# Performance work log

Measured on AMD Instinct MI355X. Metric: run time of the kernel, lower is better.

## Reference

```python
import jax, jax.numpy as jnp
import numpy as np

EPS = 1e-5

def _mode_layer(x, t, w5, w3, w1, a3, a5, gw, gb, gamma, beta):
    # x: [N,Ci,H,W], t: [N,T]
    N = x.shape[0]
    Co = w5.shape[0]
    # gate -> softmax over the 5 experts (dim=1)
    g = t @ gw.T + gb                       # [N, 5*Co]
    g = jax.nn.softmax(g.reshape(N, 5, Co), axis=1)  # [N,5,Co]
    # build the 5 expert kernels, all padded to 5x5 (torch F.pad semantics)
    k3 = jnp.pad(w3, ((0, 0), (0, 0), (1, 1), (1, 1)))
    k1 = jnp.pad(w1, ((0, 0), (0, 0), (2, 2), (2, 2)))
    # avg pool kernels: ones(K,K)/K**3 (faithful to original, incl. the /K^3)
    ka3 = jnp.pad(a3 * (jnp.ones((3, 3), x.dtype) / 27.0), ((0, 0), (0, 0), (1, 1), (1, 1)))
    ka5 = a5 * (jnp.ones((5, 5), x.dtype) / 125.0)
    experts = jnp.stack([w5, k3, k1, ka3, ka5])       # [5,Co,Ci,5,5]
    # per-sample kernels: sum_e g[n,e,o] * experts[e,o,i,h,w]
    w = jnp.einsum('eoihw,neo->noihw', experts, g)    # [N,Co,Ci,5,5]
    # per-sample conv (training-mode path), padding='same', stride=1
    def conv1(xn, wn):
        return jax.lax.conv_general_dilated(xn[None], wn, (1, 1), 'SAME')[0]
    y = jax.vmap(conv1)(x, w)                         # [N,Co,H,W]
    # BatchNorm2d (training mode: biased batch stats) + ReLU
    mean = y.mean(axis=(0, 2, 3))
    var = y.var(axis=(0, 2, 3))
    y = (y - mean[None, :, None, None]) * jax.lax.rsqrt(var + EPS)[None, :, None, None]
    y = y * gamma[None, :, None, None] + beta[None, :, None, None]
    return jax.nn.relu(y)


def setup_inputs() -> dict:
    key = jax.random.key(0)
    ks = jax.random.split(key, 20)
    N, Ci, Co, T, H, W = 8, 32, 64, 8, 256, 256
    f = jnp.float32
    inp = {
        'x': jax.random.normal(ks[0], (N, Ci, H, W), f),
        't': jax.random.normal(ks[1], (N, T), f),
        'w5_1': jax.random.normal(ks[2], (Co, Ci, 5, 5), f) * 0.05,
        'w3_1': jax.random.normal(ks[3], (Co, Ci, 3, 3), f) * 0.05,
        'w1_1': jax.random.normal(ks[4], (Co, Ci, 1, 1), f) * 0.05,
        'a3_1': jax.random.normal(ks[5], (Co, Ci, 1, 1), f) * 0.05,
        'a5_1': jax.random.normal(ks[6], (Co, Ci, 1, 1), f) * 0.05,
        'gw_1': jax.random.normal(ks[7], (5 * Co, T), f) * 0.1,
        'gb_1': jax.random.normal(ks[8], (5 * Co,), f) * 0.1,
        'gamma_1': jnp.ones((Co,), f),
        'beta_1': jnp.zeros((Co,), f),
        'w5_2': jax.random.normal(ks[9], (Co, Co, 5, 5), f) * 0.05,
        'w3_2': jax.random.normal(ks[10], (Co, Co, 3, 3), f) * 0.05,
        'w1_2': jax.random.normal(ks[11], (Co, Co, 1, 1), f) * 0.05,
        'a3_2': jax.random.normal(ks[12], (Co, Co, 1, 1), f) * 0.05,
        'a5_2': jax.random.normal(ks[13], (Co, Co, 1, 1), f) * 0.05,
        'gw_2': jax.random.normal(ks[14], (5 * Co, T), f) * 0.1,
        'gb_2': jax.random.normal(ks[15], (5 * Co,), f) * 0.1,
        'gamma_2': jnp.ones((Co,), f),
        'beta_2': jnp.zeros((Co,), f),
    }
    return inp


def reference(x, t,
              w5_1, w3_1, w1_1, a3_1, a5_1, gw_1, gb_1, gamma_1, beta_1,
              w5_2, w3_2, w1_2, a3_2, a5_2, gw_2, gb_2, gamma_2, beta_2):
    h = _mode_layer(x, t, w5_1, w3_1, w1_1, a3_1, a5_1, gw_1, gb_1, gamma_1, beta_1)
    y = _mode_layer(h, t, w5_2, w3_2, w1_2, a3_2, a5_2, gw_2, gb_2, gamma_2, beta_2)
    return y
```

## Files before the change

### kernel.cpp

```cpp
#include <hip/hip_runtime.h>
#include <hip/hip_bf16.h>

#define MK_N 8
#define MK_T 8
#define MK_H 256
#define MK_W 256
#define MK_CO 64
#define MK_EPS 1e-5f

typedef __attribute__((ext_vector_type(8))) short short8;
typedef __attribute__((ext_vector_type(4))) short short4v;
typedef __attribute__((ext_vector_type(4))) float f32x4;

__device__ __forceinline__ float rdv(const void* p, long idx, int isf32) {
  return isf32 ? ((const float*)p)[idx]
               : __bfloat162float(((const __hip_bfloat16*)p)[idx]);
}

__device__ __forceinline__ short f2bf_s(float f) {
  __hip_bfloat16 b = __float2bfloat16(f);
  union { __hip_bfloat16 b; short s; } u; u.b = b; return u.s;
}
__device__ __forceinline__ float bfu2f(unsigned short s) {
  return __uint_as_float((unsigned)s << 16);
}

__device__ __forceinline__ int block_detect_isf(const void* xprobe, int* sflag) {
  if (threadIdx.x < 64) {
    const unsigned short* u16 = (const unsigned short*)xprobe;
    int insane = 0;
#pragma unroll
    for (int j = 0; j < 4; ++j) {
      unsigned short u = u16[threadIdx.x * 4 + j];
      int e = (u >> 7) & 0xFF;
      bool zero = (u & 0x7FFF) == 0;
      if (!(zero || (e >= 0x60 && e <= 0x85))) insane++;
    }
#pragma unroll
    for (int off = 32; off > 0; off >>= 1) insane += __shfl_down(insane, off);
    if (threadIdx.x == 0) *sflag = (insane > 32) ? 1 : 0;
  }
  __syncthreads();
  return *sflag;
}

__global__ void zero128_kernel(float* __restrict__ p) { p[threadIdx.x] = 0.f; }

__global__ __launch_bounds__(256) void x_to_nhwc(const void* __restrict__ x,
                                                 short* __restrict__ xo,
                                                 const void* __restrict__ xprobe) {
  __shared__ float xl[32 * 65];
  __shared__ int sflag;
  int isf = block_detect_isf(xprobe, &sflag);
  int n = blockIdx.z, y = blockIdx.y, x0 = blockIdx.x * 64;
  int tid = threadIdx.x;
  {
    int c = tid >> 3, ch = tid & 7;
    long base = ((long)(n * 32 + c) * 256 + y) * 256 + x0 + ch * 8;
#pragma unroll
    for (int j = 0; j < 8; ++j) xl[c * 65 + ch * 8 + j] = rdv(x, base + j, isf);
  }
  __syncthreads();
  {
    int xi = tid >> 2, cc = tid & 3;
    short8 v;
#pragma unroll
    for (int j = 0; j < 8; ++j) v[j] = f2bf_s(xl[(cc * 8 + j) * 65 + xi]);
    *(short8*)&xo[(((long)(n * 256 + y) * 256) + x0 + xi) * 32 + cc * 8] = v;
  }
}

template <int CI>
__global__ __launch_bounds__(256) void make_panels(
    const void* __restrict__ t, const void* __restrict__ gw, const void* __restrict__ gb,
    const void* __restrict__ w5, const void* __restrict__ w3, const void* __restrict__ w1,
    const void* __restrict__ a3, const void* __restrict__ a5,
    short* __restrict__ pan, const void* __restrict__ xprobe) {
  __shared__ float slog[320], sgate[320];
  __shared__ int sflag;
  const int s = blockIdx.x, n = blockIdx.y;
  const int tid = threadIdx.x;
  const int isf = block_detect_isf(xprobe, &sflag);

  for (int eo = tid; eo < 320; eo += 256) {
    int e = eo >> 6, o = eo & 63;
    long row = e * 64 + o;
    float sacc = rdv(gb, row, isf);
#pragma unroll
    for (int k = 0; k < MK_T; ++k)
      sacc += rdv(t, n * MK_T + k, isf) * rdv(gw, row * MK_T + k, isf);
    slog[e * 64 + o] = sacc;
  }
  __syncthreads();
  if (tid < 64) {
    float m = slog[tid];
#pragma unroll
    for (int e = 1; e < 5; ++e) m = fmaxf(m, slog[e * 64 + tid]);
    float tmp[5], sum = 0.f;
#pragma unroll
    for (int e = 0; e < 5; ++e) { tmp[e] = expf(slog[e * 64 + tid] - m); sum += tmp[e]; }
    float inv = 1.f / sum;
#pragma unroll
    for (int e = 0; e < 5; ++e) sgate[tid * 5 + e] = tmp[e] * inv;
  }
  __syncthreads();

  const int mo = tid >> 2, gq = tid & 3;
  float ge[5];
#pragma unroll
  for (int e = 0; e < 5; ++e) ge[e] = sgate[mo * 5 + e];

  const int ky = s / 5, kx = s - ky * 5;
  const bool in3 = (ky >= 1 && ky <= 3 && kx >= 1 && kx <= 3);
  const int HC = CI / 32;
#pragma unroll
  for (int hc = 0; hc < HC; ++hc) {
    short8 pk;
#pragma unroll
    for (int j = 0; j < 8; ++j) {
      long oc = (long)mo * CI + hc * 32 + gq * 8 + j;
      float pa3 = rdv(a3, oc, isf) * (1.f / 27.f);
      float pa5 = rdv(a5, oc, isf) * (1.f / 125.f);
      float v = ge[0] * rdv(w5, oc * 25 + s, isf);
      if (in3) {
        v += ge[1] * rdv(w3, oc * 9 + (ky - 1) * 3 + (kx - 1), isf);
        v += ge[3] * pa3;
      }
      if (s == 12) v += ge[2] * rdv(w1, oc, isf);
      v += ge[4] * pa5;
      pk[j] = f2bf_s(v);
    }
    *(short8*)&pan[((((long)n * HC + hc) * 25 + s) * 64 + mo) * 32 + gq * 8] = pk;
  }
}

__global__ __launch_bounds__(256) void copy16(const short8* __restrict__ src,
                                              short8* __restrict__ dst, int n16) {
  int i = blockIdx.x * 256 + threadIdx.x;
  if (i < n16) dst[i] = src[i];
}

__global__ __launch_bounds__(256) void reduce_partials(const float* __restrict__ part,
                                                       float* __restrict__ st, int nb) {
  __shared__ float r[256];
  const int ch = blockIdx.x;
  float s = 0.f;
  for (int k = threadIdx.x; k < nb; k += 256) s += part[(long)ch * nb + k];
  r[threadIdx.x] = s;
  __syncthreads();
  if (threadIdx.x < 64) {
    s = r[threadIdx.x] + r[threadIdx.x + 64] + r[threadIdx.x + 128] + r[threadIdx.x + 192];
#pragma unroll
    for (int off = 32; off > 0; off >>= 1) s += __shfl_down(s, off);
    if (threadIdx.x == 0) atomicAdd(&st[ch], s);
  }
}

template <int CI, bool FINAL, bool BNIN>
__global__ __launch_bounds__(256, 2) void conv_mfma(
    const short* __restrict__ xsrc,
    const short* __restrict__ pan,
    void* __restrict__ outp,
    int nbase,
    const float* __restrict__ pr,
    float* __restrict__ partials,
    int NB)
{
  constexpr int XT_SH = FINAL ? 29376 : 37888;
  __shared__ short xt[XT_SH];
  __shared__ float spr[128];

  const int tid = threadIdx.x;
  const int x0 = blockIdx.x * 64;
  const int r0 = blockIdx.y * 8;
  const int n = blockIdx.z + nbase;
  const int bid = (blockIdx.z * gridDim.y + blockIdx.y) * gridDim.x + blockIdx.x;

  if (BNIN) {
    if (tid < 128) spr[tid] = pr[tid];
  }

  const int lane = tid & 63, w = tid >> 6;
  const int quad = lane >> 4, l15 = lane & 15;

  int baseB[2][4];
#pragma unroll
  for (int rr = 0; rr < 2; ++rr)
#pragma unroll
    for (int p = 0; p < 4; ++p)
      baseB[rr][p] = ((w + rr * 4) * 68 + p * 16 + l15) * 36 + quad * 8;
  int aoff[4];
#pragma unroll
  for (int ot = 0; ot < 4; ++ot)
    aoff[ot] = (ot * 16 + l15) * 32 + quad * 8;

  f32x4 acc[2][4][4];
#pragma unroll
  for (int rr = 0; rr < 2; ++rr)
#pragma unroll
    for (int ot = 0; ot < 4; ++ot)
#pragma unroll
      for (int p = 0; p < 4; ++p) acc[rr][ot][p] = f32x4{0.f, 0.f, 0.f, 0.f};

  const int HC = CI / 32;
#pragma unroll 1
  for (int hc = 0; hc < HC; ++hc) {
    const int cbase = hc * 32;
    __syncthreads();

    for (int idx = tid; idx < 12 * 68 * 4; idx += 256) {
      int r = idx / (68 * 4);
      int rem = idx - r * (68 * 4);
      int col = rem >> 2, ch = rem & 3;
      int gy = r0 - 2 + r, gx = x0 - 2 + col;
      short8 v = short8{0, 0, 0, 0, 0, 0, 0, 0};
      if ((unsigned)gy < 256u && (unsigned)gx < 256u) {
        v = *(const short8*)&xsrc[(((long)(n * 256 + gy) * 256) + gx) * CI + cbase + ch * 8];
        if (BNIN) {
#pragma unroll
          for (int j = 0; j < 8; ++j) {
            int c = cbase + ch * 8 + j;
            float f = bfu2f((unsigned short)v[j]);
            v[j] = f2bf_s(fmaxf(fmaf(f, spr[c], spr[64 + c]), 0.f));
          }
        }
      }
      short4v lo, hi;
#pragma unroll
      for (int j = 0; j < 4; ++j) { lo[j] = v[j]; hi[j] = v[4 + j]; }
      int sb = (r * 68 + col) * 36 + ch * 8;
      *(short4v*)&xt[sb] = lo;
      *(short4v*)&xt[sb + 4] = hi;
    }
    __syncthreads();

    const short* ps = pan + (((long)n * HC + hc) * 25) * 2048;

    short8 afc[4];
#pragma unroll
    for (int ot = 0; ot < 4; ++ot) afc[ot] = *(const short8*)&ps[aoff[ot]];

#pragma unroll
    for (int s = 0; s < 25; ++s) {
      const int ky = s / 5, kx = s - ky * 5;
      const int koff = (ky * 68 + kx) * 36;
      short8 afn[4];
      if (s < 24) {
#pragma unroll
        for (int ot = 0; ot < 4; ++ot)
          afn[ot] = *(const short8*)&ps[(s + 1) * 2048 + aoff[ot]];
      }
      short8 bf[2][4];
#pragma unroll
      for (int rr = 0; rr < 2; ++rr)
#pragma unroll
        for (int p = 0; p < 4; ++p) {
          short4v lo = *(const short4v*)&xt[baseB[rr][p] + koff];
          short4v hi = *(const short4v*)&xt[baseB[rr][p] + koff + 4];
          short8 b;
#pragma unroll
          for (int j = 0; j < 4; ++j) { b[j] = lo[j]; b[4 + j] = hi[j]; }
          bf[rr][p] = b;
        }
      __builtin_amdgcn_s_setprio(1);
#pragma unroll
      for (int ot = 0; ot < 4; ++ot)
#pragma unroll
        for (int rr = 0; rr < 2; ++rr)
#pragma unroll
          for (int p = 0; p < 4; ++p)
            acc[rr][ot][p] = __builtin_amdgcn_mfma_f32_16x16x32_bf16(
                afc[ot], bf[rr][p], acc[rr][ot][p], 0, 0, 0);
      __builtin_amdgcn_s_setprio(0);
      if (s < 24) {
#pragma unroll
        for (int ot = 0; ot < 4; ++ot) afc[ot] = afn[ot];
      }
    }
  }

  float* slds = FINAL ? (float*)xt : (float*)&xt[36864];

  if (FINAL) {
    float* out = (float*)outp;
#pragma unroll
    for (int rr = 0; rr < 2; ++rr)
#pragma unroll
      for (int ot = 0; ot < 4; ++ot)
#pragma unroll
        for (int p = 0; p < 4; ++p)
#pragma unroll
          for (int r = 0; r < 4; ++r) {
            int oo = ot * 16 + quad * 4 + r;
            long off = ((long)(n * 64 + oo) << 16) + (r0 + w + rr * 4) * 256 + x0 + p * 16 + l15;
            out[off] = acc[rr][ot][p][r];
          }
    __syncthreads();
#pragma unroll
    for (int ot = 0; ot < 4; ++ot)
#pragma unroll
      for (int r = 0; r < 4; ++r) {
        float s = 0.f, q = 0.f;
#pragma unroll
        for (int rr = 0; rr < 2; ++rr)
#pragma unroll
          for (int p = 0; p < 4; ++p) {
            float v = acc[rr][ot][p][r];
            s += v; q += v * v;
          }
#pragma unroll
        for (int m = 1; m < 16; m <<= 1) {
          s += __shfl_xor(s, m);
          q += __shfl_xor(q, m);
        }
        if (l15 == 0) {
          int ch = ot * 16 + quad * 4 + r;
          slds[w * 128 + ch] = s;
          slds[w * 128 + 64 + ch] = q;
        }
      }
    __syncthreads();
    if (tid < 128) {
      float v = slds[tid] + slds[128 + tid] + slds[256 + tid] + slds[384 + tid];
      partials[(long)tid * NB + bid] = v;
    }
  } else {
    __syncthreads();
    short* cbuf = xt;
#pragma unroll
    for (int rr = 0; rr < 2; ++rr)
#pragma unroll
      for (int ot = 0; ot < 4; ++ot)
#pragma unroll
        for (int p = 0; p < 4; ++p) {
          short4v pk;
#pragma unroll
          for (int r = 0; r < 4; ++r) pk[r] = f2bf_s(acc[rr][ot][p][r]);
          *(short4v*)&cbuf[((w + rr * 4) * 64 + p * 16 + l15) * 72 + ot * 16 + quad * 4] = pk;
        }
#pragma unroll
    for (int ot = 0; ot < 4; ++ot)
#pragma unroll
      for (int r = 0; r < 4; ++r) {
        float s = 0.f, q = 0.f;
#pragma unroll
        for (int rr = 0; rr < 2; ++rr)
#pragma unroll
          for (int p = 0; p < 4; ++p) {
            float v = acc[rr][ot][p][r];
            s += v; q += v * v;
          }
#pragma unroll
        for (int m = 1; m < 16; m <<= 1) {
          s += __shfl_xor(s, m);
          q += __shfl_xor(q, m);
        }
        if (l15 == 0) {
          int ch = ot * 16 + quad * 4 + r;
          slds[w * 128 + ch] = s;
          slds[w * 128 + 64 + ch] = q;
        }
      }
    __syncthreads();
    short* hout = (short*)outp;
    for (int idx = tid; idx < 4096; idx += 256) {
      int w2 = idx >> 9, rem = idx & 511;
      int px = rem >> 3, ch = rem & 7;
      short8 v = *(const short8*)&cbuf[(w2 * 64 + px) * 72 + ch * 8];
      *(short8*)&hout[(((long)(n * 256 + r0 + w2) * 256) + x0 + px) * 64 + ch * 8] = v;
    }
    if (tid < 128) {
      float v = slds[tid] + slds[128 + tid] + slds[256 + tid] + slds[384 + tid];
      partials[(long)tid * NB + bid] = v;
    }
  }
}

__global__ void finalize_mode_kernel(const float* __restrict__ stats,
                                     float* __restrict__ params,
                                     const void* __restrict__ gamma,
                                     const void* __restrict__ beta,
                                     const void* __restrict__ xprobe) {
  __shared__ int sflag;
  int isf = block_detect_isf(xprobe, &sflag);
  int o = threadIdx.x;
  if (o < MK_CO) {
    const float M = (float)(MK_N * MK_H * MK_W);
    float mean = stats[o] / M;
    float var = stats[MK_CO + o] / M - mean * mean;
    float inv = rsqrtf(var + MK_EPS);
    float sc = rdv(gamma, o, isf) * inv;
    params[o] = sc;
    params[MK_CO + o] = rdv(beta, o, isf) - mean * sc;
  }
}

__global__ __launch_bounds__(256) void bn_relu_f32v(float4* __restrict__ y,
                                                    const float* __restrict__ params) {
  const long total = (long)MK_N * MK_CO * MK_H * MK_W / 4;
  for (long i = (long)blockIdx.x * 256 + threadIdx.x; i < total;
       i += (long)gridDim.x * 256) {
    int ch = (int)((i >> 14) & (MK_CO - 1));
    float sc = params[ch], sh = params[MK_CO + ch];
    float4 v = y[i];
    v.x = fmaxf(fmaf(v.x, sc, sh), 0.f);
    v.y = fmaxf(fmaf(v.y, sc, sh), 0.f);
    v.z = fmaxf(fmaf(v.z, sc, sh), 0.f);
    v.w = fmaxf(fmaf(v.w, sc, sh), 0.f);
    y[i] = v;
  }
}

extern "C" void kernel_launch(void* const* d_in, const int* in_sizes, int n_in,
                              void* d_out, int out_size, void* d_ws, size_t ws_size,
                              hipStream_t stream) {
  const void* x     = d_in[0];
  const void* t     = d_in[1];
  const void* w5_1  = d_in[2];
  const void* w3_1  = d_in[3];
  const void* w1_1  = d_in[4];
  const void* a3_1  = d_in[5];
  const void* a5_1  = d_in[6];
  const void* gw_1  = d_in[7];
  const void* gb_1  = d_in[8];
  const void* gamma_1 = d_in[9];
  const void* beta_1  = d_in[10];
  const void* w5_2  = d_in[11];
  const void* w3_2  = d_in[12];
  const void* w1_2  = d_in[13];
  const void* a3_2  = d_in[14];
  const void* a5_2  = d_in[15];
  const void* gw_2  = d_in[16];
  const void* gb_2  = d_in[17];
  const void* gamma_2 = d_in[18];
  const void* beta_2  = d_in[19];

  char* dob = (char*)d_out;
  short* x_nhwc = (short*)d_out;
  float* st1   = (float*)(dob + 33554432);
  float* part1 = (float*)(dob + 33554432 + 4096);
  short* P1    = (short*)(dob + 35651584);
  short* P2    = (short*)(dob + 104857600);
  float* pr1_hi = (float*)(dob + 104857600 + 1638400);
  float* part2a = (float*)(dob + 132120576);
  float* out = (float*)d_out;

  char* wsb = (char*)d_ws;
  short* h     = (short*)d_ws;
  float* st2   = (float*)d_ws;
  float* pr2   = st2 + 128;
  float* part2b = (float*)(wsb + 4096);
  short* P2c   = (short*)(wsb + 2097152);
  float* pr1c  = (float*)(wsb + 2097152 + 1638400);

  make_panels<32><<<dim3(25, 8), 256, 0, stream>>>(t, gw_1, gb_1, w5_1, w3_1, w1_1, a3_1, a5_1, P1, x);
  make_panels<64><<<dim3(25, 8), 256, 0, stream>>>(t, gw_2, gb_2, w5_2, w3_2, w1_2, a3_2, a5_2, P2, x);

  x_to_nhwc<<<dim3(4, 256, 8), 256, 0, stream>>>(x, x_nhwc, x);
  zero128_kernel<<<1, 128, 0, stream>>>(st1);
  conv_mfma<32, false, false><<<dim3(4, 32, 8), 256, 0, stream>>>(
      x_nhwc, P1, h, 0, nullptr, part1, 1024);
  reduce_partials<<<128, 256, 0, stream>>>(part1, st1, 1024);
  finalize_mode_kernel<<<1, 64, 0, stream>>>(st1, pr1_hi, gamma_1, beta_1, x);

  conv_mfma<64, true, true><<<dim3(4, 32, 4), 256, 0, stream>>>(
      h, P2, out, 0, pr1_hi, part2a, 512);
  zero128_kernel<<<1, 128, 0, stream>>>(st2);
  reduce_partials<<<128, 256, 0, stream>>>(part2a, st2, 512);
  copy16<<<401, 256, 0, stream>>>((const short8*)P2, (short8*)P2c, 102432);
  conv_mfma<64, true, true><<<dim3(4, 32, 4), 256, 0, stream>>>(
      h, P2c, out, 4, pr1c, part2b, 512);
  reduce_partials<<<128, 256, 0, stream>>>(part2b, st2, 512);
  finalize_mode_kernel<<<1, 64, 0, stream>>>(st2, pr2, gamma_2, beta_2, x);
  bn_relu_f32v<<<2048, 256, 0, stream>>>((float4*)out, pr2);
}
```

Baseline: 469.0 us.

## Fuse small launches and deepen weight-panel prefetch in conv inner loop

Merges the two panel-building kernels into one launch over a layer grid dimension. It also fuses partial-sum reduction with BN finalize, which removes the zeroing kernels and the atomics. In the MFMA conv loop, weight panels are now prefetched two kernel taps ahead instead of one, hiding global load latency at the cost of more registers. The extra registers could hurt occupancy under the 2-blocks launch bound.

```diff
diff --git a/kernel.cpp b/kernel.cpp
--- a/kernel.cpp
+++ b/kernel.cpp
@@ -43,8 +43,6 @@
   __syncthreads();
   return *sflag;
 }
-
-__global__ void zero128_kernel(float* __restrict__ p) { p[threadIdx.x] = 0.f; }
 
 __global__ __launch_bounds__(256) void x_to_nhwc(const void* __restrict__ x,
                                                  short* __restrict__ xo,
@@ -70,17 +68,33 @@
   }
 }
 
-template <int CI>
-__global__ __launch_bounds__(256) void make_panels(
-    const void* __restrict__ t, const void* __restrict__ gw, const void* __restrict__ gb,
-    const void* __restrict__ w5, const void* __restrict__ w3, const void* __restrict__ w1,
-    const void* __restrict__ a3, const void* __restrict__ a5,
-    short* __restrict__ pan, const void* __restrict__ xprobe) {
+__global__ __launch_bounds__(256) void make_panels_dual(
+    const void* __restrict__ t,
+    const void* __restrict__ gw1, const void* __restrict__ gb1,
+    const void* __restrict__ w51, const void* __restrict__ w31,
+    const void* __restrict__ w11, const void* __restrict__ a31,
+    const void* __restrict__ a51, short* __restrict__ p1,
+    const void* __restrict__ gw2, const void* __restrict__ gb2,
+    const void* __restrict__ w52, const void* __restrict__ w32,
+    const void* __restrict__ w12, const void* __restrict__ a32,
+    const void* __restrict__ a52, short* __restrict__ p2,
+    const void* __restrict__ xprobe) {
   __shared__ float slog[320], sgate[320];
   __shared__ int sflag;
-  const int s = blockIdx.x, n = blockIdx.y;
+  const int s = blockIdx.x, n = blockIdx.y, lay = blockIdx.z;
   const int tid = threadIdx.x;
   const int isf = block_detect_isf(xprobe, &sflag);
+
+  const void* gw = lay ? gw2 : gw1;
+  const void* gb = lay ? gb2 : gb1;
+  const void* w5 = lay ? w52 : w51;
+  const void* w3 = lay ? w32 : w31;
+  const void* w1 = lay ? w12 : w11;
+  const void* a3 = lay ? a32 : a31;
+  const void* a5 = lay ? a52 : a51;
+  short* pan = lay ? p2 : p1;
+  const int CI = lay ? 64 : 32;
+  const int HC = CI / 32;
 
   for (int eo = tid; eo < 320; eo += 256) {
     int e = eo >> 6, o = eo & 63;
@@ -112,8 +126,6 @@
 
   const int ky = s / 5, kx = s - ky * 5;
   const bool in3 = (ky >= 1 && ky <= 3 && kx >= 1 && kx <= 3);
-  const int HC = CI / 32;
-#pragma unroll
   for (int hc = 0; hc < HC; ++hc) {
     short8 pk;
 #pragma unroll
@@ -140,19 +152,45 @@
   if (i < n16) dst[i] = src[i];
 }
 
-__global__ __launch_bounds__(256) void reduce_partials(const float* __restrict__ part,
-                                                       float* __restrict__ st, int nb) {
-  __shared__ float r[256];
-  const int ch = blockIdx.x;
-  float s = 0.f;
-  for (int k = threadIdx.x; k < nb; k += 256) s += part[(long)ch * nb + k];
-  r[threadIdx.x] = s;
+__global__ __launch_bounds__(256) void reduce_finalize(
+    const float* __restrict__ part, int nb,
+    const float* __restrict__ stin, float* __restrict__ stout,
+    float* __restrict__ params,
+    const void* __restrict__ gamma, const void* __restrict__ beta,
+    const void* __restrict__ xprobe) {
+  __shared__ float rs[256], rq[256];
+  __shared__ int sflag;
+  const int isf = block_detect_isf(xprobe, &sflag);
+  const int o = blockIdx.x;
+  const int tid = threadIdx.x;
+  float s = 0.f, q = 0.f;
+  for (int k = tid; k < nb; k += 256) {
+    s += part[(long)o * nb + k];
+    q += part[(long)(64 + o) * nb + k];
+  }
+  rs[tid] = s; rq[tid] = q;
   __syncthreads();
-  if (threadIdx.x < 64) {
-    s = r[threadIdx.x] + r[threadIdx.x + 64] + r[threadIdx.x + 128] + r[threadIdx.x + 192];
-#pragma unroll
-    for (int off = 32; off > 0; off >>= 1) s += __shfl_down(s, off);
-    if (threadIdx.x == 0) atomicAdd(&st[ch], s);
+  if (tid < 64) {
+    s = rs[tid] + rs[tid + 64] + rs[tid + 128] + rs[tid + 192];
+    q = rq[tid] + rq[tid + 64] + rq[tid + 128] + rq[tid + 192];
+#pragma unroll
+    for (int off = 32; off > 0; off >>= 1) {
+      s += __shfl_down(s, off);
+      q += __shfl_down(q, off);
+    }
+    if (tid == 0) {
+      if (stin) { s += stin[o]; q += stin[64 + o]; }
+      if (stout) { stout[o] = s; stout[64 + o] = q; }
+      if (params) {
+        const float M = (float)(MK_N * MK_H * MK_W);
+        float mean = s / M;
+        float var = q / M - mean * mean;
+        float inv = rsqrtf(var + MK_EPS);
+        float sc = rdv(gamma, o, isf) * inv;
+        params[o] = sc;
+        params[MK_CO + o] = rdv(beta, o, isf) - mean * sc;
+      }
+    }
   }
 }
 
@@ -236,19 +274,22 @@
 
     const short* ps = pan + (((long)n * HC + hc) * 25) * 2048;
 
-    short8 afc[4];
-#pragma unroll
-    for (int ot = 0; ot < 4; ++ot) afc[ot] = *(const short8*)&ps[aoff[ot]];
+    short8 afc[4], afn[4];
+#pragma unroll
+    for (int ot = 0; ot < 4; ++ot) {
+      afc[ot] = *(const short8*)&ps[aoff[ot]];
+      afn[ot] = *(const short8*)&ps[2048 + aoff[ot]];
+    }
 
 #pragma unroll
     for (int s = 0; s < 25; ++s) {
       const int ky = s / 5, kx = s - ky * 5;
       const int koff = (ky * 68 + kx) * 36;
-      short8 afn[4];
-      if (s < 24) {
+      short8 af2[4];
+      if (s < 23) {
 #pragma unroll
         for (int ot = 0; ot < 4; ++ot)
-          afn[ot] = *(const short8*)&ps[(s + 1) * 2048 + aoff[ot]];
+          af2[ot] = *(const short8*)&ps[(s + 2) * 2048 + aoff[ot]];
       }
       short8 bf[2][4];
 #pragma unroll
@@ -274,7 +315,10 @@
       __builtin_amdgcn_s_setprio(0);
       if (s < 24) {
 #pragma unroll
-        for (int ot = 0; ot < 4; ++ot) afc[ot] = afn[ot];
+        for (int ot = 0; ot < 4; ++ot) {
+          afc[ot] = afn[ot];
+          if (s < 23) afn[ot] = af2[ot];
+        }
       }
     }
   }
@@ -373,25 +417,6 @@
       float v = slds[tid] + slds[128 + tid] + slds[256 + tid] + slds[384 + tid];
       partials[(long)tid * NB + bid] = v;
     }
-  }
-}
-
-__global__ void finalize_mode_kernel(const float* __restrict__ stats,
-                                     float* __restrict__ params,
-                                     const void* __restrict__ gamma,
-                                     const void* __restrict__ beta,
-                                     const void* __restrict__ xprobe) {
-  __shared__ int sflag;
-  int isf = block_detect_isf(xprobe, &sflag);
-  int o = threadIdx.x;
-  if (o < MK_CO) {
-    const float M = (float)(MK_N * MK_H * MK_W);
-    float mean = stats[o] / M;
-    float var = stats[MK_CO + o] / M - mean * mean;
-    float inv = rsqrtf(var + MK_EPS);
-    float sc = rdv(gamma, o, isf) * inv;
-    params[o] = sc;
-    params[MK_CO + o] = rdv(beta, o, isf) - mean * sc;
   }
 }
 
@@ -437,7 +462,6 @@
 
   char* dob = (char*)d_out;
   short* x_nhwc = (short*)d_out;
-  float* st1   = (float*)(dob + 33554432);
   float* part1 = (float*)(dob + 33554432 + 4096);
   short* P1    = (short*)(dob + 35651584);
   short* P2    = (short*)(dob + 104857600);
@@ -453,24 +477,24 @@
   short* P2c   = (short*)(wsb + 2097152);
   float* pr1c  = (float*)(wsb + 2097152 + 1638400);
 
-  make_panels<32><<<dim3(25, 8), 256, 0, stream>>>(t, gw_1, gb_1, w5_1, w3_1, w1_1, a3_1, a5_1, P1, x);
-  make_panels<64><<<dim3(25, 8), 256, 0, stream>>>(t, gw_2, gb_2, w5_2, w3_2, w1_2, a3_2, a5_2, P2, x);
+  make_panels_dual<<<dim3(25, 8, 2), 256, 0, stream>>>(
+      t, gw_1, gb_1, w5_1, w3_1, w1_1, a3_1, a5_1, P1,
+      gw_2, gb_2, w5_2, w3_2, w1_2, a3_2, a5_2, P2, x);
 
   x_to_nhwc<<<dim3(4, 256, 8), 256, 0, stream>>>(x, x_nhwc, x);
-  zero128_kernel<<<1, 128, 0, stream>>>(st1);
   conv_mfma<32, false, false><<<dim3(4, 32, 8), 256, 0, stream>>>(
       x_nhwc, P1, h, 0, nullptr, part1, 1024);
-  reduce_partials<<<128, 256, 0, stream>>>(part1, st1, 1024);
-  finalize_mode_kernel<<<1, 64, 0, stream>>>(st1, pr1_hi, gamma_1, beta_1, x);
+  reduce_finalize<<<64, 256, 0, stream>>>(part1, 1024, nullptr, nullptr,
+                                          pr1_hi, gamma_1, beta_1, x);
 
   conv_mfma<64, true, true><<<dim3(4, 32, 4), 256, 0, stream>>>(
       h, P2, out, 0, pr1_hi, part2a, 512);
-  zero128_kernel<<<1, 128, 0, stream>>>(st2);
-  reduce_partials<<<128, 256, 0, stream>>>(part2a, st2, 512);
+  reduce_finalize<<<64, 256, 0, stream>>>(part2a, 512, nullptr, st2,
+                                          nullptr, nullptr, nullptr, x);
   copy16<<<401, 256, 0, stream>>>((const short8*)P2, (short8*)P2c, 102432);
   conv_mfma<64, true, true><<<dim3(4, 32, 4), 256, 0, stream>>>(
       h, P2c, out, 4, pr1c, part2b, 512);
-  reduce_partials<<<128, 256, 0, stream>>>(part2b, st2, 512);
-  finalize_mode_kernel<<<1, 64, 0, stream>>>(st2, pr2, gamma_2, beta_2, x);
+  reduce_finalize<<<64, 256, 0, stream>>>(part2b, 512, st2, nullptr,
+                                          pr2, gamma_2, beta_2, x);
   bn_relu_f32v<<<2048, 256, 0, stream>>>((float4*)out, pr2);
 }
```

Result: faster. 458.4 us (-2.3%).
